# Optimization experiments

Measured on AMD Instinct MI355X. Metric: run time of the kernel, lower is better.

Reference implementation:

```python
import jax, jax.numpy as jnp
import numpy as np
import itertools

B, H, W, C = 64, 28, 28, 576
NH, WS = 18, 7
KD = C // NH          # head dim = 32 (attn_ratio=1 so d == key_dim)
HID = 4 * C           # mlp hidden
N = WS * WS           # tokens per window = 49


def _bias_idxs():
    points = list(itertools.product(range(WS), range(WS)))
    offsets, idxs = {}, []
    for p1 in points:
        for p2 in points:
            off = (abs(p1[0] - p2[0]), abs(p1[1] - p2[1]))
            if off not in offsets:
                offsets[off] = len(offsets)
            idxs.append(offsets[off])
    return np.asarray(idxs, dtype=np.int64).reshape(N, N), len(offsets)


def setup_inputs() -> dict:
    key = jax.random.key(0)
    ks = jax.random.split(key, 10)
    idxs, n_off = _bias_idxs()  # n_off == 49
    s = 0.02
    return {
        "x": jax.random.normal(ks[0], (B, H * W, C), jnp.float32),
        "gamma_a": jnp.ones((C,), jnp.float32),
        "beta_a": jnp.zeros((C,), jnp.float32),
        "qkv_w": jax.random.normal(ks[1], (3 * C, C), jnp.float32) * s,
        "qkv_b": jnp.zeros((3 * C,), jnp.float32),
        "proj_w": jax.random.normal(ks[2], (C, C), jnp.float32) * s,
        "proj_b": jnp.zeros((C,), jnp.float32),
        "attn_biases": jax.random.normal(ks[3], (NH, n_off), jnp.float32) * s,
        "conv_w": jax.random.normal(ks[4], (C, 1, 3, 3), jnp.float32) * 0.1,
        "bn_gamma": jnp.ones((C,), jnp.float32),
        "bn_beta": jnp.zeros((C,), jnp.float32),
        "bn_mean": jnp.zeros((C,), jnp.float32),
        "bn_var": jax.random.uniform(ks[5], (C,), jnp.float32, 0.5, 1.5),
        "gamma_m": jnp.ones((C,), jnp.float32),
        "beta_m": jnp.zeros((C,), jnp.float32),
        "fc1_w": jax.random.normal(ks[6], (HID, C), jnp.float32) * s,
        "fc1_b": jnp.zeros((HID,), jnp.float32),
        "fc2_w": jax.random.normal(ks[7], (C, HID), jnp.float32) * s,
        "fc2_b": jnp.zeros((C,), jnp.float32),
        "bias_idxs": jnp.asarray(idxs),
    }


def _ln(x, g, b, eps=1e-5):
    mu = x.mean(-1, keepdims=True)
    var = ((x - mu) ** 2).mean(-1, keepdims=True)
    return (x - mu) * jax.lax.rsqrt(var + eps) * g + b


def reference(x, gamma_a, beta_a, qkv_w, qkv_b, proj_w, proj_b, attn_biases,
              conv_w, bn_gamma, bn_beta, bn_mean, bn_var,
              gamma_m, beta_m, fc1_w, fc1_b, fc2_w, fc2_b, bias_idxs):
    scale = KD ** -0.5
    nWh, nWw = H // WS, W // WS
    res = x
    # ---- window partition: (B, H*W, C) -> (B*nWh*nWw, 49, C) ----
    xw = x.reshape(B, nWh, WS, nWw, WS, C).transpose(0, 1, 3, 2, 4, 5)
    xw = xw.reshape(-1, N, C)
    # ---- windowed attention with gathered relative-position bias ----
    h = _ln(xw, gamma_a, beta_a)
    qkv = h @ qkv_w.T + qkv_b                       # (Bw, N, 3C)
    qkv = qkv.reshape(-1, N, NH, 3 * KD)
    q, k, v = jnp.split(qkv, 3, axis=-1)            # each (Bw, N, NH, KD)
    q = q.transpose(0, 2, 1, 3)
    k = k.transpose(0, 2, 1, 3)
    v = v.transpose(0, 2, 1, 3)
    bias = attn_biases[:, bias_idxs]                # (NH, N, N)
    attn = jnp.einsum('bhnd,bhmd->bhnm', q, k) * scale + bias
    attn = jax.nn.softmax(attn, axis=-1)
    out = jnp.einsum('bhnm,bhmd->bhnd', attn, v)    # (Bw, NH, N, KD)
    out = out.transpose(0, 2, 1, 3).reshape(-1, N, C) @ proj_w.T + proj_b
    # ---- window reverse ----
    out = out.reshape(B, nWh, nWw, WS, WS, C).transpose(0, 1, 3, 2, 4, 5)
    out = out.reshape(B, H * W, C)
    x = res + out
    # ---- depthwise 3x3 conv + BatchNorm (inference stats) ----
    xc = x.transpose(0, 2, 1).reshape(B, C, H, W)
    xc = jax.lax.conv_general_dilated(
        xc, conv_w, (1, 1), [(1, 1), (1, 1)],
        feature_group_count=C,
        dimension_numbers=('NCHW', 'OIHW', 'NCHW'))
    eps = 1e-5
    inv = (jax.lax.rsqrt(bn_var + eps) * bn_gamma)[:, None, None]
    xc = (xc - bn_mean[:, None, None]) * inv + bn_beta[:, None, None]
    x = xc.reshape(B, C, H * W).transpose(0, 2, 1)
    # ---- MLP with pre-LayerNorm ----
    hm = _ln(x, gamma_m, beta_m)
    hm = jax.nn.gelu(hm @ fc1_w.T + fc1_b, approximate=False)
    hm = hm @ fc2_w.T + fc2_b
    return x + hm
```

## Files before the change

### kernel.cpp

```cpp
#include <hip/hip_runtime.h>
#include <hip/hip_bf16.h>

typedef __bf16 v8bf  __attribute__((ext_vector_type(8)));
typedef __bf16 v4bf  __attribute__((ext_vector_type(4)));
typedef float  f32x4 __attribute__((ext_vector_type(4)));
typedef float  f32x8 __attribute__((ext_vector_type(8)));

#define TOKENS 50176
#define CDIM   576
#define NHEAD  18
#define QKVD   1728

__device__ __forceinline__ void gld16(const __bf16* g, __bf16* l)
{
    __builtin_amdgcn_global_load_lds(
        (const __attribute__((address_space(1))) void*)g,
        (__attribute__((address_space(3))) void*)l,
        16, 0, 0);
}

__global__ __launch_bounds__(256)
void cast_kernel(const float* __restrict__ in, __bf16* __restrict__ out)
{
    const size_t i = ((size_t)blockIdx.x * 256 + threadIdx.x) * 4;
    f32x4 v = *(const f32x4*)&in[i];
    v4bf o;
#pragma unroll
    for (int j = 0; j < 4; ++j) o[j] = (__bf16)v[j];
    *(v4bf*)&out[i] = o;
}

__global__ __launch_bounds__(64)
void conv_prep(const float* __restrict__ w, const float* __restrict__ bg,
               const float* __restrict__ bb, const float* __restrict__ bm,
               const float* __restrict__ bv, __bf16* __restrict__ wt,
               float* __restrict__ bias2)
{
    const int c = blockIdx.x * 64 + threadIdx.x;
    const float inv = rsqrtf(bv[c] + 1e-5f) * bg[c];
#pragma unroll
    for (int t = 0; t < 9; ++t) wt[t * CDIM + c] = (__bf16)(w[c * 9 + t] * inv);
    bias2[c] = bb[c] - bm[c] * inv;
}

template<typename InT>
__global__ __launch_bounds__(256)
void ln_kernel(const InT* __restrict__ x, const float* __restrict__ g,
               const float* __restrict__ b, __bf16* __restrict__ out)
{
    const int lane = threadIdx.x & 63;
    const int wid  = threadIdx.x >> 6;
    const size_t t = (size_t)blockIdx.x * 4 + wid;
    const InT* row = x + t * CDIM;

    float v[16];
    float sum = 0.f, sq = 0.f;
    if constexpr (sizeof(InT) == 2) {
        v8bf d0 = *(const v8bf*)&row[(size_t)lane * 8];
#pragma unroll
        for (int j = 0; j < 8; ++j) { float f = (float)d0[j]; v[j] = f; sum += f; sq += f * f; }
    } else {
        f32x8 d0 = *(const f32x8*)&row[(size_t)lane * 8];
#pragma unroll
        for (int j = 0; j < 8; ++j) { float f = d0[j]; v[j] = f; sum += f; sq += f * f; }
    }
    if (lane < 8) {
        if constexpr (sizeof(InT) == 2) {
            v8bf d1 = *(const v8bf*)&row[(size_t)(lane + 64) * 8];
#pragma unroll
            for (int j = 0; j < 8; ++j) { float f = (float)d1[j]; v[8 + j] = f; sum += f; sq += f * f; }
        } else {
            f32x8 d1 = *(const f32x8*)&row[(size_t)(lane + 64) * 8];
#pragma unroll
            for (int j = 0; j < 8; ++j) { float f = d1[j]; v[8 + j] = f; sum += f; sq += f * f; }
        }
    }
#pragma unroll
    for (int o = 32; o >= 1; o >>= 1) {
        sum += __shfl_xor(sum, o, 64);
        sq  += __shfl_xor(sq,  o, 64);
    }
    const float mean = sum * (1.0f / CDIM);
    const float rstd = rsqrtf(sq * (1.0f / CDIM) - mean * mean + 1e-5f);

    {
        int c0 = lane * 8;
        v8bf o0;
#pragma unroll
        for (int j = 0; j < 8; ++j)
            o0[j] = (__bf16)((v[j] - mean) * rstd * g[c0 + j] + b[c0 + j]);
        *(v8bf*)&out[t * CDIM + c0] = o0;
    }
    if (lane < 8) {
        int c0 = (lane + 64) * 8;
        v8bf o1;
#pragma unroll
        for (int j = 0; j < 8; ++j)
            o1[j] = (__bf16)((v[8 + j] - mean) * rstd * g[c0 + j] + b[c0 + j]);
        *(v8bf*)&out[t * CDIM + c0] = o1;
    }
}

template<int EPI, typename OutT, typename AddT>
__global__ __launch_bounds__(256)
void gemm_bt(const __bf16* __restrict__ A, const __bf16* __restrict__ W,
             const float* __restrict__ bias, const AddT* __restrict__ add,
             OutT* __restrict__ C, int N, int K, int nN)
{
    constexpr int BM = 256, BN = 64, BK = 32;
    __shared__ __bf16 As[BM][BK];
    __shared__ __bf16 Ws[BN][BK];
    const int tid = threadIdx.x, lane = tid & 63, wid = tid >> 6;
    const int lr = lane & 15, kh = lane >> 4;

    const int nwg = gridDim.x, bid = blockIdx.x;
    const int q = nwg >> 3, r = nwg & 7;
    const int xcd = bid & 7, j = bid >> 3;
    const int wgid = (xcd < r ? xcd * (q + 1) : r * (q + 1) + (xcd - r) * q) + j;
    const int mblk = wgid / nN, nblk = wgid - mblk * nN;
    const int m0 = mblk * BM, n0 = nblk * BN;

    const int rsub = lane >> 2;
    const int cgs  = ((lane & 3) ^ (rsub & 3)) * 8;
    const __bf16* pA = A + (size_t)(m0 + wid * 64 + rsub) * K + cgs;
    const __bf16* pW = W + (size_t)(n0 + wid * 16 + rsub) * K + cgs;
    __bf16* lA = &As[wid * 64][0];
    __bf16* lW = &Ws[wid * 16][0];

    f32x4 acc[4][4] = {};

    for (int k0 = 0; k0 < K; k0 += BK) {
        __syncthreads();
#pragma unroll
        for (int i = 0; i < 4; ++i)
            gld16(pA + (size_t)i * 16 * K + k0, lA + i * 16 * BK);
        gld16(pW + k0, lW);
        __syncthreads();

        v8bf a[4], b[4];
#pragma unroll
        for (int m = 0; m < 4; ++m) {
            int rr = wid * 64 + m * 16 + lr;
            a[m] = *(const v8bf*)&As[rr][(kh ^ (rr & 3)) * 8];
        }
#pragma unroll
        for (int n = 0; n < 4; ++n) {
            int rr = n * 16 + lr;
            b[n] = *(const v8bf*)&Ws[rr][(kh ^ (rr & 3)) * 8];
        }
#pragma unroll
        for (int m = 0; m < 4; ++m)
#pragma unroll
            for (int n = 0; n < 4; ++n)
                acc[m][n] = __builtin_amdgcn_mfma_f32_16x16x32_bf16(a[m], b[n], acc[m][n], 0, 0, 0);
    }

#pragma unroll
    for (int m = 0; m < 4; ++m)
#pragma unroll
        for (int n = 0; n < 4; ++n)
#pragma unroll
            for (int rr = 0; rr < 4; ++rr) {
                int row = m0 + wid * 64 + m * 16 + kh * 4 + rr;
                int col = n0 + n * 16 + lr;
                float vv = acc[m][n][rr] + bias[col];
                if (EPI == 1) vv += (float)add[(size_t)row * N + col];
                if (EPI == 2) vv = 0.5f * vv * (1.0f + erff(vv * 0.70710678118654752f));
                C[(size_t)row * N + col] = (OutT)vv;
            }
}

__global__ __launch_bounds__(64)
void attn_kernel(const __bf16* __restrict__ qkv, const float* __restrict__ biases,
                 const int* __restrict__ bidx, __bf16* __restrict__ out)
{
    const int head = blockIdx.x;
    const int win  = blockIdx.y;
    const int tid  = threadIdx.x;
    const int b  = win >> 4;
    const int wy = (win >> 2) & 3;
    const int wx = win & 3;
    __shared__ float kk[49][32];
    __shared__ float vv[49][32];
    const size_t hb = (size_t)head * 96;

    for (int e = tid; e < 49 * 32; e += 64) {
        int n = e >> 5, d = e & 31;
        int iy = n / 7, ix = n - iy * 7;
        size_t t = (size_t)b * 784 + (size_t)(wy * 7 + iy) * 28 + wx * 7 + ix;
        const __bf16* p = qkv + t * QKVD + hb;
        kk[n][d] = (float)p[32 + d];
        vv[n][d] = (float)p[64 + d];
    }
    float q[32];
    size_t tmine = 0;
    if (tid < 49) {
        int iy = tid / 7, ix = tid - iy * 7;
        tmine = (size_t)b * 784 + (size_t)(wy * 7 + iy) * 28 + wx * 7 + ix;
        const __bf16* p = qkv + tmine * QKVD + hb;
#pragma unroll
        for (int d = 0; d < 32; ++d) q[d] = (float)p[d];
    }
    __syncthreads();
    if (tid >= 49) return;

    const float scale = 0.17677669529663687f;
    float s[49];
    float mx = -1e30f;
    const int*   brow = bidx + tid * 49;
    const float* bh   = biases + head * 49;
#pragma unroll
    for (int m = 0; m < 49; ++m) {
        float dot = 0.f;
#pragma unroll
        for (int d = 0; d < 32; ++d) dot += q[d] * kk[m][d];
        float val = dot * scale + bh[brow[m]];
        s[m] = val;
        mx = fmaxf(mx, val);
    }
    float sum = 0.f;
#pragma unroll
    for (int m = 0; m < 49; ++m) { float e = __expf(s[m] - mx); s[m] = e; sum += e; }
    const float rs = 1.0f / sum;

    __bf16* op = out + tmine * CDIM + (size_t)head * 32;
#pragma unroll
    for (int d = 0; d < 32; ++d) {
        float a = 0.f;
#pragma unroll
        for (int m = 0; m < 49; ++m) a += s[m] * vv[m][d];
        op[d] = (__bf16)(a * rs);
    }
}

__global__ __launch_bounds__(256)
void conv_bn_v(const __bf16* __restrict__ xin, const __bf16* __restrict__ wt,
               const float* __restrict__ bias2, __bf16* __restrict__ xout)
{
    const size_t gt = (size_t)blockIdx.x * 256 + threadIdx.x;
    const int g = (int)(gt % 72);
    const size_t p = gt / 72;
    const int bimg = (int)(p / 784);
    const int pix  = (int)(p - (size_t)bimg * 784);
    const int y = pix / 28, xx = pix - y * 28;
    const int c0 = g * 8;

    float acc[8];
    {
        f32x4 b0 = *(const f32x4*)&bias2[c0];
        f32x4 b1 = *(const f32x4*)&bias2[c0 + 4];
#pragma unroll
        for (int jj = 0; jj < 4; ++jj) { acc[jj] = b0[jj]; acc[4 + jj] = b1[jj]; }
    }
#pragma unroll
    for (int dy = 0; dy < 3; ++dy) {
        int ny = y + dy - 1;
        if (ny < 0 || ny >= 28) continue;
#pragma unroll
        for (int dx = 0; dx < 3; ++dx) {
            int nx = xx + dx - 1;
            if (nx < 0 || nx >= 28) continue;
            v8bf xv = *(const v8bf*)&xin[((size_t)bimg * 784 + ny * 28 + nx) * CDIM + c0];
            v8bf wv = *(const v8bf*)&wt[(dy * 3 + dx) * CDIM + c0];
#pragma unroll
            for (int jj = 0; jj < 8; ++jj) acc[jj] += (float)xv[jj] * (float)wv[jj];
        }
    }
    v8bf o;
#pragma unroll
    for (int jj = 0; jj < 8; ++jj) o[jj] = (__bf16)acc[jj];
    *(v8bf*)&xout[p * CDIM + c0] = o;
}

extern "C" void kernel_launch(void* const* d_in, const int* in_sizes, int n_in,
                              void* d_out, int out_size, void* d_ws, size_t ws_size,
                              hipStream_t stream)
{
    (void)in_sizes; (void)n_in; (void)out_size; (void)ws_size;
    const float* x          = (const float*)d_in[0];
    const float* gamma_a    = (const float*)d_in[1];
    const float* beta_a     = (const float*)d_in[2];
    const float* qkv_w      = (const float*)d_in[3];
    const float* qkv_b      = (const float*)d_in[4];
    const float* proj_w     = (const float*)d_in[5];
    const float* proj_b     = (const float*)d_in[6];
    const float* attn_bias  = (const float*)d_in[7];
    const float* conv_w     = (const float*)d_in[8];
    const float* bn_g       = (const float*)d_in[9];
    const float* bn_b       = (const float*)d_in[10];
    const float* bn_m       = (const float*)d_in[11];
    const float* bn_v       = (const float*)d_in[12];
    const float* gamma_m    = (const float*)d_in[13];
    const float* beta_m     = (const float*)d_in[14];
    const float* fc1_w      = (const float*)d_in[15];
    const float* fc1_b      = (const float*)d_in[16];
    const float* fc2_w      = (const float*)d_in[17];
    const float* fc2_b      = (const float*)d_in[18];
    const int*   bidx       = (const int*)d_in[19];

    const size_t T = TOKENS;
    __bf16* ws     = (__bf16*)d_ws;
    __bf16* hbuf   = ws;
    __bf16* qkvbuf = ws + T * 576;
    __bf16* aout   = ws;
    __bf16* x2     = ws + T * 2304;
    __bf16* x3     = x2 + T * 576;
    __bf16* lnm    = x2;
    __bf16* f1     = ws;
    __bf16* wq     = x3 + T * 576;
    __bf16* wp     = wq + (size_t)QKVD * CDIM;
    __bf16* w1     = wp + (size_t)CDIM * CDIM;
    __bf16* w2     = w1 + (size_t)2304 * CDIM;
    __bf16* wt     = w2 + (size_t)CDIM * 2304;
    float*  bias2  = (float*)(wt + 9 * CDIM);
    float*  outp   = (float*)d_out;

    cast_kernel<<<dim3((QKVD * CDIM) / 1024), 256, 0, stream>>>(qkv_w, wq);
    cast_kernel<<<dim3((CDIM * CDIM) / 1024), 256, 0, stream>>>(proj_w, wp);
    cast_kernel<<<dim3((2304 * CDIM) / 1024), 256, 0, stream>>>(fc1_w, w1);
    cast_kernel<<<dim3((CDIM * 2304) / 1024), 256, 0, stream>>>(fc2_w, w2);
    conv_prep<<<dim3(9), 64, 0, stream>>>(conv_w, bn_g, bn_b, bn_m, bn_v, wt, bias2);

    ln_kernel<float><<<dim3(T / 4), 256, 0, stream>>>(x, gamma_a, beta_a, hbuf);
    gemm_bt<0, __bf16, float><<<dim3(196 * 27), 256, 0, stream>>>(
        hbuf, wq, qkv_b, nullptr, qkvbuf, QKVD, CDIM, 27);
    attn_kernel<<<dim3(NHEAD, 1024), 64, 0, stream>>>(qkvbuf, attn_bias, bidx, aout);
    gemm_bt<1, __bf16, float><<<dim3(196 * 9), 256, 0, stream>>>(
        aout, wp, proj_b, x, x2, CDIM, CDIM, 9);
    conv_bn_v<<<dim3(14112), 256, 0, stream>>>(x2, wt, bias2, x3);
    ln_kernel<__bf16><<<dim3(T / 4), 256, 0, stream>>>(x3, gamma_m, beta_m, lnm);
    gemm_bt<2, __bf16, float><<<dim3(196 * 36), 256, 0, stream>>>(
        lnm, w1, fc1_b, nullptr, f1, 2304, CDIM, 36);
    gemm_bt<1, float, __bf16><<<dim3(196 * 9), 256, 0, stream>>>(
        f1, w2, fc2_b, x3, outp, CDIM, 2304, 9);
}
```

Measured before the change: 1.094 ms.

## Double-buffer LDS tiles in bf16 GEMM with lane-major layout

The GEMM kernel now keeps two LDS buffers for the A and W tiles. It issues the direct-to-LDS global loads for the next K step before running the MFMAs on the current one, so only one barrier per iteration remains instead of two. The LDS tile layout changes to a lane-major 16x(4x8) block arrangement that matches the MFMA operand reads, which removes the XOR swizzle. A minimum-occupancy hint of four blocks is added to launch bounds. The cost is double the LDS per block, and the occupancy hint may constrain register allocation.

```diff
diff --git a/kernel.cpp b/kernel.cpp
--- a/kernel.cpp
+++ b/kernel.cpp
@@ -102,14 +102,14 @@
 }
 
 template<int EPI, typename OutT, typename AddT>
-__global__ __launch_bounds__(256)
+__global__ __launch_bounds__(256, 4)
 void gemm_bt(const __bf16* __restrict__ A, const __bf16* __restrict__ W,
              const float* __restrict__ bias, const AddT* __restrict__ add,
              OutT* __restrict__ C, int N, int K, int nN)
 {
     constexpr int BM = 256, BN = 64, BK = 32;
-    __shared__ __bf16 As[BM][BK];
-    __shared__ __bf16 Ws[BN][BK];
+    __shared__ __bf16 As[2][BM * BK];
+    __shared__ __bf16 Ws[2][BN * BK];
     const int tid = threadIdx.x, lane = tid & 63, wid = tid >> 6;
     const int lr = lane & 15, kh = lane >> 4;
 
@@ -120,39 +120,44 @@
     const int mblk = wgid / nN, nblk = wgid - mblk * nN;
     const int m0 = mblk * BM, n0 = nblk * BN;
 
-    const int rsub = lane >> 2;
-    const int cgs  = ((lane & 3) ^ (rsub & 3)) * 8;
-    const __bf16* pA = A + (size_t)(m0 + wid * 64 + rsub) * K + cgs;
-    const __bf16* pW = W + (size_t)(n0 + wid * 16 + rsub) * K + cgs;
-    __bf16* lA = &As[wid * 64][0];
-    __bf16* lW = &Ws[wid * 16][0];
+    const __bf16* pA = A + (size_t)(m0 + wid * 64 + lr) * K + kh * 8;
+    const __bf16* pW = W + (size_t)(n0 + wid * 16 + lr) * K + kh * 8;
+
+    auto stage = [&](int s, int kk) {
+#pragma unroll
+        for (int i = 0; i < 4; ++i)
+            gld16(pA + (size_t)(i * 16) * K + kk, &As[s][(wid * 4 + i) * 512]);
+        gld16(pW + kk, &Ws[s][wid * 512]);
+    };
+
+    const int rdA = (wid * 256 + kh * 16 + lr) * 8;
+    const int rdB = (kh * 16 + lr) * 8;
 
     f32x4 acc[4][4] = {};
 
-    for (int k0 = 0; k0 < K; k0 += BK) {
-        __syncthreads();
-#pragma unroll
-        for (int i = 0; i < 4; ++i)
-            gld16(pA + (size_t)i * 16 * K + k0, lA + i * 16 * BK);
-        gld16(pW + k0, lW);
-        __syncthreads();
+    const int nk = K / BK;
+    stage(0, 0);
+    __syncthreads();
+
+    int cur = 0;
+    for (int t = 0; t < nk; ++t) {
+        if (t + 1 < nk) stage(cur ^ 1, (t + 1) * BK);
 
         v8bf a[4], b[4];
 #pragma unroll
-        for (int m = 0; m < 4; ++m) {
-            int rr = wid * 64 + m * 16 + lr;
-            a[m] = *(const v8bf*)&As[rr][(kh ^ (rr & 3)) * 8];
-        }
-#pragma unroll
-        for (int n = 0; n < 4; ++n) {
-            int rr = n * 16 + lr;
-            b[n] = *(const v8bf*)&Ws[rr][(kh ^ (rr & 3)) * 8];
-        }
+        for (int m = 0; m < 4; ++m) a[m] = *(const v8bf*)&As[cur][rdA + m * 512];
+#pragma unroll
+        for (int n = 0; n < 4; ++n) b[n] = *(const v8bf*)&Ws[cur][rdB + n * 512];
 #pragma unroll
         for (int m = 0; m < 4; ++m)
 #pragma unroll
             for (int n = 0; n < 4; ++n)
                 acc[m][n] = __builtin_amdgcn_mfma_f32_16x16x32_bf16(a[m], b[n], acc[m][n], 0, 0, 0);
+
+        if (t + 1 < nk) {
+            __syncthreads();
+            cur ^= 1;
+        }
     }
 
 #pragma unroll
```

New measurement: 1.270 ms. 1.16x slower.
